# Optimization experiments

Hardware: AMD Instinct MI355X
Metric: run time of the kernel (lower is better)

The kernel has to match this reference:

```python
import jax, jax.numpy as jnp
import numpy as np

B, C = 1048576, 32
NEG_WEIGHT = 1.0
EPS = 1e-7


def setup_inputs() -> dict:
    key = jax.random.key(0)
    k1, k2 = jax.random.split(key)
    logits = jax.random.normal(k1, (B, C), dtype=jnp.float32)
    target = jax.random.uniform(k2, (B, C), dtype=jnp.float32)
    return {"logits": logits, "target": target}


def reference(logits, target):
    # pred = clamp(sigmoid(logits), eps, 1-eps)
    pred = jnp.clip(jax.nn.sigmoid(logits), EPS, 1.0 - EPS)
    logp = jnp.log(pred)          # [B, C]
    log1mp = jnp.log(1.0 - pred)  # [B, C]

    labels = jnp.argmax(target, axis=1)  # [B]

    # Branch label == 0: mean over classes of full soft-BCE
    loss0 = jnp.mean(target * logp + (1.0 - target) * log1mp, axis=1)  # [B]

    # Branch label != 0: target[i,label]*log(pred[i,label]) + neg_w*log(1-pred[i,0])
    rows = jnp.arange(target.shape[0])
    t_lab = target[rows, labels]
    logp_lab = logp[rows, labels]
    loss1 = t_lab * logp_lab + NEG_WEIGHT * log1mp[:, 0]  # [B]

    per_row = jnp.where(labels == 0, loss0, loss1)  # [B]
    # reduction == 'mean'
    return -jnp.mean(per_row)
```

## Files before the change

kernel.cpp:

```cpp
#include <hip/hip_runtime.h>
#include <math.h>


#define LOG_EPS   -16.118095651f
#define LOG_1MEPS -1.1920929e-07f

__global__ void zero_out_kernel(float* out) { out[0] = 0.0f; }

__device__ __forceinline__ void elem(float x, float t, int col,
                                     float& rs, float& bv, int& bi,
                                     float& lpmax, float& l1p0)
{
    float e   = __builtin_exp2f(x * -1.44269504f);
    float lpu = __builtin_log2f(1.0f + e) * -0.69314718f;
    float lp  = fminf(fmaxf(lpu,     LOG_EPS), LOG_1MEPS);
    float l1p = fminf(fmaxf(lpu - x, LOG_EPS), LOG_1MEPS);
    rs = fmaf(t, lp - l1p, rs + l1p);
    if (col == 0) l1p0 = l1p;
    if (t > bv) { bv = t; bi = col; lpmax = lp; }
}

__global__ __launch_bounds__(256) void softbce_kernel(
    const float* __restrict__ logits,
    const float* __restrict__ target,
    float* __restrict__ out,
    int B)
{
    const int row = blockIdx.x * 256 + threadIdx.x;

    float acc = 0.0f;
    if (row < B) {
        const float4* tg = (const float4*)target + (size_t)row * 8;
        const float4* lg = (const float4*)logits + (size_t)row * 8;

        float4 T[8], X[8];
        #pragma unroll
        for (int j = 0; j < 8; ++j) T[j] = tg[j];
        #pragma unroll
        for (int j = 0; j < 8; ++j) X[j] = lg[j];

        float rs = 0.0f, bv = -INFINITY, lpmax = 0.0f, l1p0 = 0.0f;
        int   bi = 0;
        #pragma unroll
        for (int j = 0; j < 8; ++j) {
            elem(X[j].x, T[j].x, 4*j + 0, rs, bv, bi, lpmax, l1p0);
            elem(X[j].y, T[j].y, 4*j + 1, rs, bv, bi, lpmax, l1p0);
            elem(X[j].z, T[j].z, 4*j + 2, rs, bv, bi, lpmax, l1p0);
            elem(X[j].w, T[j].w, 4*j + 3, rs, bv, bi, lpmax, l1p0);
        }

        acc = (bi == 0) ? rs * (1.0f / 32.0f) : fmaf(bv, lpmax, l1p0);
    }

    #pragma unroll
    for (int d = 1; d < 64; d <<= 1) acc += __shfl_xor(acc, d);

    __shared__ float sacc[4];
    const int lane = threadIdx.x & 63;
    if (lane == 0) sacc[threadIdx.x >> 6] = acc;
    __syncthreads();
    if (threadIdx.x == 0) {
        float s = sacc[0] + sacc[1] + sacc[2] + sacc[3];
        atomicAdd(out, s * (-1.0f / (float)B));
    }
}

extern "C" void kernel_launch(void* const* d_in, const int* in_sizes, int n_in,
                              void* d_out, int out_size, void* d_ws, size_t ws_size,
                              hipStream_t stream) {
    const float* logits = (const float*)d_in[0];
    const float* target = (const float*)d_in[1];
    float* out = (float*)d_out;

    const int B = in_sizes[0] / 32;

    zero_out_kernel<<<1, 1, 0, stream>>>(out);
    softbce_kernel<<<(B + 255) / 256, 256, 0, stream>>>(logits, target, out, B);
}
```

Baseline: 282.2 us.

## Split each row across four lanes with DPP reductions and grid-stride loop

Each row is now handled by a quad of four lanes, each loading 8 contiguous floats, so the wave's global loads are coalesced instead of every thread reading a whole 128-byte row. Row sum, argmax with lowest-index tie-break, and the column-0 term are combined across the quad with DPP quad-permute moves. The launch becomes a fixed 2048-block persistent grid-stride loop. The math drops the eps clamps and folds the ln2 scaling into the final atomic, which can change results for extreme logits.

```diff
diff --git a/kernel.cpp b/kernel.cpp
--- a/kernel.cpp
+++ b/kernel.cpp
@@ -2,22 +2,23 @@
 #include <math.h>
 
 
-#define LOG_EPS   -16.118095651f
-#define LOG_1MEPS -1.1920929e-07f
+#define LOG2E 1.44269504088896340736f
+#define LN2   0.69314718055994530942f
+
+#define QP_XOR1   0xB1
+#define QP_XOR2   0x4E
+#define QP_BCAST0 0x00
 
 __global__ void zero_out_kernel(float* out) { out[0] = 0.0f; }
 
-__device__ __forceinline__ void elem(float x, float t, int col,
-                                     float& rs, float& bv, int& bi,
-                                     float& lpmax, float& l1p0)
-{
-    float e   = __builtin_exp2f(x * -1.44269504f);
-    float lpu = __builtin_log2f(1.0f + e) * -0.69314718f;
-    float lp  = fminf(fmaxf(lpu,     LOG_EPS), LOG_1MEPS);
-    float l1p = fminf(fmaxf(lpu - x, LOG_EPS), LOG_1MEPS);
-    rs = fmaf(t, lp - l1p, rs + l1p);
-    if (col == 0) l1p0 = l1p;
-    if (t > bv) { bv = t; bi = col; lpmax = lp; }
+template <int CTRL>
+__device__ __forceinline__ float dppf(float v) {
+    return __int_as_float(
+        __builtin_amdgcn_mov_dpp(__float_as_int(v), CTRL, 0xF, 0xF, true));
+}
+template <int CTRL>
+__device__ __forceinline__ int dppi(int v) {
+    return __builtin_amdgcn_mov_dpp(v, CTRL, 0xF, 0xF, true);
 }
 
 __global__ __launch_bounds__(256) void softbce_kernel(
@@ -26,42 +27,69 @@
     float* __restrict__ out,
     int B)
 {
-    const int row = blockIdx.x * 256 + threadIdx.x;
+    const int lane = threadIdx.x & 63;
+    const int sub  = lane & 3;
+    const int wid  = (blockIdx.x * 256 + threadIdx.x) >> 6;
+    const int nw   = (gridDim.x * 256) >> 6;
+    const int nIter = B >> 4;
+    const int colBase = sub * 8;
 
     float acc = 0.0f;
-    if (row < B) {
-        const float4* tg = (const float4*)target + (size_t)row * 8;
-        const float4* lg = (const float4*)logits + (size_t)row * 8;
 
-        float4 T[8], X[8];
-        #pragma unroll
-        for (int j = 0; j < 8; ++j) T[j] = tg[j];
-        #pragma unroll
-        for (int j = 0; j < 8; ++j) X[j] = lg[j];
+    for (int c = wid; c < nIter; c += nw) {
+        const size_t r = (size_t)c * 16 + (lane >> 2);
+        const float4* tp = (const float4*)target + r * 8 + sub * 2;
+        const float4* xp = (const float4*)logits + r * 8 + sub * 2;
+        float4 T0 = tp[0], T1 = tp[1];
+        float4 X0 = xp[0], X1 = xp[1];
 
-        float rs = 0.0f, bv = -INFINITY, lpmax = 0.0f, l1p0 = 0.0f;
-        int   bi = 0;
+        float tv[8] = {T0.x,T0.y,T0.z,T0.w,T1.x,T1.y,T1.z,T1.w};
+        float xv[8] = {X0.x,X0.y,X0.z,X0.w,X1.x,X1.y,X1.z,X1.w};
+
+        float rs = 0.0f;
+        float bv = -1.0f;
+        int   bc = 99;
+        float bl = 0.0f;
+        float z0 = 0.0f;
+
         #pragma unroll
         for (int j = 0; j < 8; ++j) {
-            elem(X[j].x, T[j].x, 4*j + 0, rs, bv, bi, lpmax, l1p0);
-            elem(X[j].y, T[j].y, 4*j + 1, rs, bv, bi, lpmax, l1p0);
-            elem(X[j].z, T[j].z, 4*j + 2, rs, bv, bi, lpmax, l1p0);
-            elem(X[j].w, T[j].w, 4*j + 3, rs, bv, bi, lpmax, l1p0);
+            float x  = xv[j], t = tv[j];
+            float t1 = -x * LOG2E;
+            float lg = __builtin_log2f(1.0f + __builtin_exp2f(t1));
+            float s1 = t1 - lg;
+            rs = fmaf(-t, t1, rs + s1);
+            if (j == 0) z0 = s1;
+            if (t > bv) { bv = t; bc = colBase + j; bl = -lg; }
         }
 
-        acc = (bi == 0) ? rs * (1.0f / 32.0f) : fmaf(bv, lpmax, l1p0);
+        rs += dppf<QP_XOR1>(rs);
+        rs += dppf<QP_XOR2>(rs);
+        {
+            float ov = dppf<QP_XOR1>(bv); int oc = dppi<QP_XOR1>(bc); float ol = dppf<QP_XOR1>(bl);
+            bool tk = (ov > bv) || (ov == bv && oc < bc);
+            bv = tk ? ov : bv; bc = tk ? oc : bc; bl = tk ? ol : bl;
+        }
+        {
+            float ov = dppf<QP_XOR2>(bv); int oc = dppi<QP_XOR2>(bc); float ol = dppf<QP_XOR2>(bl);
+            bool tk = (ov > bv) || (ov == bv && oc < bc);
+            bv = tk ? ov : bv; bc = tk ? oc : bc; bl = tk ? ol : bl;
+        }
+        float z0b = dppf<QP_BCAST0>(z0);
+
+        float loss = (bc == 0) ? rs * (1.0f / 32.0f) : fmaf(bv, bl, z0b);
+        acc += loss;
     }
 
     #pragma unroll
     for (int d = 1; d < 64; d <<= 1) acc += __shfl_xor(acc, d);
 
     __shared__ float sacc[4];
-    const int lane = threadIdx.x & 63;
-    if (lane == 0) sacc[threadIdx.x >> 6] = acc;
+    if ((threadIdx.x & 63) == 0) sacc[threadIdx.x >> 6] = acc;
     __syncthreads();
     if (threadIdx.x == 0) {
         float s = sacc[0] + sacc[1] + sacc[2] + sacc[3];
-        atomicAdd(out, s * (-1.0f / (float)B));
+        atomicAdd(out, s * (-LN2 / (4.0f * (float)B)));
     }
 }
 
@@ -75,5 +103,5 @@
     const int B = in_sizes[0] / 32;
 
     zero_out_kernel<<<1, 1, 0, stream>>>(out);
-    softbce_kernel<<<(B + 255) / 256, 256, 0, stream>>>(logits, target, out, B);
+    softbce_kernel<<<2048, 256, 0, stream>>>(logits, target, out, B);
 }
```

After: 277.3 us. About the same (-1.8%).
